# Kernel optimization log

Hardware: AMD Instinct MI355X
Metric: run time of the kernel (lower is better)

Reference implementation:

```python
import jax, jax.numpy as jnp
import numpy as np

B, S, D, H = 4, 2048, 1024, 16
HD = D // H  # head_dim = 64


def setup_inputs() -> dict:
    key = jax.random.key(0)
    ks = jax.random.split(key, 5)
    scale = 1.0 / np.sqrt(D)  # xavier-ish
    return {
        "query": jax.random.normal(ks[0], (B, S, D), dtype=jnp.float32),
        "Wq": jax.random.normal(ks[1], (D, D), dtype=jnp.float32) * scale,
        "bq": jnp.zeros((D,), dtype=jnp.float32),
        "Wk": jax.random.normal(ks[2], (D, D), dtype=jnp.float32) * scale,
        "bk": jnp.zeros((D,), dtype=jnp.float32),
        "Wv": jax.random.normal(ks[3], (D, D), dtype=jnp.float32) * scale,
        "bv": jnp.zeros((D,), dtype=jnp.float32),
        "Wo": jax.random.normal(ks[4], (D, D), dtype=jnp.float32) * scale,
        "bo": jnp.zeros((D,), dtype=jnp.float32),
    }


def reference(query, Wq, bq, Wk, bk, Wv, bv, Wo, bo):
    # Self-attention: key = value = query. Linear layers use y = x @ W^T + b (torch nn.Linear).
    q = query @ Wq.T + bq
    k = query @ Wk.T + bk
    v = query @ Wv.T + bv
    # [B, S, D] -> [B, H, S, HD]
    q = q.reshape(B, S, H, HD).transpose(0, 2, 1, 3)
    k = k.reshape(B, S, H, HD).transpose(0, 2, 1, 3)
    v = v.reshape(B, S, H, HD).transpose(0, 2, 1, 3)
    scores = jnp.einsum('bhqd,bhkd->bhqk', q, k) / jnp.sqrt(jnp.float32(HD))
    attn = jax.nn.softmax(scores, axis=-1)  # dropout=0 (eval)
    out = jnp.einsum('bhqk,bhkd->bhqd', attn, v)
    out = out.transpose(0, 2, 1, 3).reshape(B, S, D)
    out = out @ Wo.T + bo
    return out
```

## Files before the change

### kernel.cpp

```cpp
#include <hip/hip_runtime.h>
#include <cstdint>


#define B_ 4
#define S_ 2048
#define D_ 1024
#define H_ 16
#define HD_ 64
#define QKV_N 3072
#define QK_LD 2048
#define SCALE_Q 0.18033688011111772f

typedef __bf16 bf16x8 __attribute__((ext_vector_type(8)));
typedef __bf16 bf16x2 __attribute__((ext_vector_type(2)));
typedef float f32x4 __attribute__((ext_vector_type(4)));
typedef short short8 __attribute__((ext_vector_type(8)));

__device__ __forceinline__ unsigned short f2bf(float f) {
  unsigned int u = __builtin_bit_cast(unsigned int, f);
  u = (u + 0x7FFFu + ((u >> 16) & 1u)) >> 16;
  return (unsigned short)u;
}

__device__ __forceinline__ unsigned int pkbf(float a, float b) {
  bf16x2 v;
  v.x = (__bf16)a;
  v.y = (__bf16)b;
  return __builtin_bit_cast(unsigned int, v);
}

__device__ __forceinline__ void gload16(const void* g, void* l) {
  __builtin_amdgcn_global_load_lds(
      (const __attribute__((address_space(1))) void*)g,
      (__attribute__((address_space(3))) void*)l, 16, 0, 0);
}

__global__ __launch_bounds__(256) void cvt_all(
    const float* __restrict__ x, const float* __restrict__ w0, const float* __restrict__ w1,
    const float* __restrict__ w2, const float* __restrict__ w3,
    const float* __restrict__ bq, const float* __restrict__ bk, const float* __restrict__ bv,
    unsigned short* __restrict__ xb, unsigned short* __restrict__ wcat,
    float* __restrict__ bcat) {
  const int blk = blockIdx.x;
  const int t = threadIdx.x;
  if (blk < 4096) {
    size_t i = (size_t)blk * 256 + t;
    const float4* p = (const float4*)x + i * 2;
    float4 a = p[0], b = p[1];
    unsigned short o[8] = {f2bf(a.x), f2bf(a.y), f2bf(a.z), f2bf(a.w),
                           f2bf(b.x), f2bf(b.y), f2bf(b.z), f2bf(b.w)};
    *(uint4*)(xb + i * 8) = *(const uint4*)o;
  } else if (blk < 6144) {
    int y = (blk - 4096) >> 9;
    const float* src = (y == 0) ? w0 : (y == 1) ? w1 : (y == 2) ? w2 : w3;
    float s = (y == 0) ? SCALE_Q : 1.0f;
    size_t i = (size_t)((blk - 4096) & 511) * 256 + t;
    const float4* p = (const float4*)src + i * 2;
    float4 a = p[0], b = p[1];
    unsigned short o[8] = {f2bf(a.x * s), f2bf(a.y * s), f2bf(a.z * s), f2bf(a.w * s),
                           f2bf(b.x * s), f2bf(b.y * s), f2bf(b.z * s), f2bf(b.w * s)};
    *(uint4*)(wcat + (size_t)y * 1048576 + i * 8) = *(const uint4*)o;
  } else {
    for (int i = t; i < 3072; i += 256) {
      float v = (i < 1024) ? bq[i] * SCALE_Q : (i < 2048) ? bk[i - 1024] : bv[i - 2048];
      bcat[i] = v;
    }
  }
}

__device__ __forceinline__ void ld_afrag(const unsigned short* s, int rowbase, int quad,
                                         int sw, bf16x8 af[4][2]) {
#pragma unroll
  for (int mi2 = 0; mi2 < 4; ++mi2) {
    int row = rowbase + mi2 * 16;
#pragma unroll
    for (int kk = 0; kk < 2; ++kk)
      af[mi2][kk] = *(const bf16x8*)&s[row * 64 + ((((kk << 2) + quad) ^ sw) << 3)];
  }
}

__device__ __forceinline__ void ld_bfrag(const unsigned short* s, int rowbase, int quad,
                                         int sw, bf16x8 bf[2][2]) {
#pragma unroll
  for (int ni2 = 0; ni2 < 2; ++ni2) {
    int row = rowbase + ni2 * 16;
#pragma unroll
    for (int kk = 0; kk < 2; ++kk)
      bf[ni2][kk] = *(const bf16x8*)&s[row * 64 + ((((kk << 2) + quad) ^ sw) << 3)];
  }
}

#define SBAR() __builtin_amdgcn_sched_barrier(0)
#define BARRIER()                      \
  do {                                 \
    SBAR();                            \
    __builtin_amdgcn_s_barrier();      \
    SBAR();                            \
  } while (0)
#define WAITLGKM()                                      \
  do {                                                  \
    asm volatile("s_waitcnt lgkmcnt(0)" ::: "memory");  \
    SBAR();                                             \
  } while (0)

#define MM(qm, qn, BF)                                                                   \
  _Pragma("unroll") for (int mi2 = 0; mi2 < 4; ++mi2)                                    \
  _Pragma("unroll") for (int ni2 = 0; ni2 < 2; ++ni2)                                    \
  _Pragma("unroll") for (int kk = 0; kk < 2; ++kk)                                       \
      acc[(qm) * 4 + mi2][(qn) * 2 + ni2] = __builtin_amdgcn_mfma_f32_16x16x32_bf16(     \
          af[mi2][kk], BF[ni2][kk], acc[(qm) * 4 + mi2][(qn) * 2 + ni2], 0, 0, 0);

__global__ __launch_bounds__(512, 2) void gemm_qkv_256(
    const unsigned short* __restrict__ A, const unsigned short* __restrict__ W,
    const float* __restrict__ bias, unsigned short* __restrict__ qk,
    unsigned short* __restrict__ vt) {
  __shared__ __attribute__((aligned(16))) unsigned short sA[2][256 * 64];
  __shared__ __attribute__((aligned(16))) unsigned short sB[2][256 * 64];

  const int t = threadIdx.x;
  const int lane = t & 63;
  const int w = t >> 6;
  const int lm = lane & 15;
  const int quad = lane >> 4;
  const int sw = lm & 7;
  const int wm = (w >> 2) * 128;
  const int wn = (w & 3) * 64;

  const int bid = blockIdx.x;
  const int xcd = bid & 7, lin = bid >> 3;
  const int mt = xcd * 4 + (lin & 3);
  const int nt = lin >> 2;
  const int m0 = mt * 256, n0 = nt * 256;
  const int K = 1024;

  const int srow = t >> 3;
  const int scol = ((t & 7) ^ ((t >> 3) & 7)) << 3;
  const unsigned short* Ab = A + ((size_t)m0 + srow) * K + scol;
  const unsigned short* Wb = W + ((size_t)n0 + srow) * K + scol;

#define STG_A(bb, q, kt) gload16(Ab + (size_t)((q) * 64) * K + (kt), &sA[bb][(q) * 4096 + w * 512])
#define STG_B(bb, q, kt) gload16(Wb + (size_t)((q) * 64) * K + (kt), &sB[bb][(q) * 4096 + w * 512])

  STG_A(0, 0, 0); STG_A(0, 1, 0); STG_A(0, 2, 0); STG_A(0, 3, 0);
  STG_B(0, 0, 0); STG_B(0, 1, 0); STG_B(0, 2, 0); STG_B(0, 3, 0);
  STG_A(1, 0, 64); STG_A(1, 2, 64);
  STG_B(1, 0, 64); STG_B(1, 1, 64);
  STG_A(1, 1, 64); STG_A(1, 3, 64);
  asm volatile("s_waitcnt vmcnt(6)" ::: "memory");
  BARRIER();

  f32x4 acc[8][4] = {};
  bf16x8 af[4][2], bf0[2][2], bf1[2][2];

#define GROUP(c, kn1, kn2)                                                            \
  do {                                                                                \
    ld_afrag(sA[c], wm + lm, quad, sw, af);                                           \
    ld_bfrag(sB[c], wn + lm, quad, sw, bf0);                                          \
    STG_B(c ^ 1, 2, kn1);                                                             \
    STG_B(c ^ 1, 3, kn1);                                                             \
    BARRIER(); WAITLGKM();                                                            \
    __builtin_amdgcn_s_setprio(1); MM(0, 0, bf0); __builtin_amdgcn_s_setprio(0);      \
    BARRIER();                                                                        \
    ld_bfrag(sB[c], wn + 32 + lm, quad, sw, bf1);                                     \
    STG_A(c, 0, kn2);                                                                 \
    STG_A(c, 2, kn2);                                                                 \
    BARRIER(); WAITLGKM();                                                            \
    __builtin_amdgcn_s_setprio(1); MM(0, 1, bf1); __builtin_amdgcn_s_setprio(0);      \
    BARRIER();                                                                        \
    ld_afrag(sA[c], wm + 64 + lm, quad, sw, af);                                      \
    STG_B(c, 0, kn2);                                                                 \
    STG_B(c, 1, kn2);                                                                 \
    BARRIER(); WAITLGKM();                                                            \
    __builtin_amdgcn_s_setprio(1); MM(1, 0, bf0); __builtin_amdgcn_s_setprio(0);      \
    BARRIER();                                                                        \
    STG_A(c, 1, kn2);                                                                 \
    STG_A(c, 3, kn2);                                                                 \
    asm volatile("s_waitcnt vmcnt(6)" ::: "memory");                                  \
    BARRIER();                                                                        \
    __builtin_amdgcn_s_setprio(1); MM(1, 1, bf1); __builtin_amdgcn_s_setprio(0);      \
    BARRIER();                                                                        \
  } while (0)

  for (int kt = 0; kt < K; kt += 128) {
    const int kn1a = kt + 64;
    const int kn2a = (kt + 128 < K) ? kt + 128 : K - 64;
    const int kn1b = kn2a;
    const int kn2b = (kt + 192 < K) ? kt + 192 : K - 64;
    GROUP(0, kn1a, kn2a);
    GROUP(1, kn1b, kn2b);
  }

  asm volatile("s_waitcnt vmcnt(0)" ::: "memory");

#pragma unroll
  for (int mi = 0; mi < 8; ++mi) {
    const int rbase = m0 + wm + mi * 16 + quad * 4;
#pragma unroll
    for (int ni = 0; ni < 4; ++ni) {
      const int col = n0 + wn + ni * 16 + lm;
      const float bv = bias[col];
      float v0 = acc[mi][ni][0] + bv, v1 = acc[mi][ni][1] + bv;
      float v2 = acc[mi][ni][2] + bv, v3 = acc[mi][ni][3] + bv;
      if (n0 < 2048) {
        qk[(size_t)(rbase + 0) * QK_LD + col] = f2bf(v0);
        qk[(size_t)(rbase + 1) * QK_LD + col] = f2bf(v1);
        qk[(size_t)(rbase + 2) * QK_LD + col] = f2bf(v2);
        qk[(size_t)(rbase + 3) * QK_LD + col] = f2bf(v3);
      } else {
        int c2 = col - 2048;
        int bh = (m0 >> 11) * 16 + (c2 >> 6);
        int hd = c2 & 63;
        int sbase = rbase & 2047;
        uint2 pk = {pkbf(v0, v1), pkbf(v2, v3)};
        *(uint2*)(vt + (size_t)bh * (HD_ * S_) + (size_t)hd * S_ + sbase) = pk;
      }
    }
  }
}

__global__ __launch_bounds__(256) void gemm_bt(
    const unsigned short* __restrict__ A, const unsigned short* __restrict__ W,
    const float* __restrict__ bias, void* __restrict__ Cout,
    unsigned short* __restrict__ vt, int M, int N, int K, int mode) {
  __shared__ __attribute__((aligned(16))) unsigned short sA[128 * 32];
  __shared__ __attribute__((aligned(16))) unsigned short sB[128 * 32];
  const int t = threadIdx.x;
  const int lane = t & 63;
  const int w = t >> 6;
  const int lm = lane & 15;
  const int quad = lane >> 4;
  const int m0 = blockIdx.x * 128;
  const int n0 = blockIdx.y * 128;
  const int wm = (w & 1) * 64;
  const int wn = (w >> 1) * 64;

  const int off0 = t * 8, off1 = t * 8 + 2048;
  const int ar0 = off0 >> 5, ac0 = (((off0 >> 3) & 3) ^ ((ar0 >> 1) & 3)) * 8;
  const int ar1 = off1 >> 5, ac1 = (((off1 >> 3) & 3) ^ ((ar1 >> 1) & 3)) * 8;
  const unsigned short* Ag0 = A + (size_t)(m0 + ar0) * K + ac0;
  const unsigned short* Ag1 = A + (size_t)(m0 + ar1) * K + ac1;
  const unsigned short* Wg0 = W + (size_t)(n0 + ar0) * K + ac0;
  const unsigned short* Wg1 = W + (size_t)(n0 + ar1) * K + ac1;
  unsigned short* sA0 = &sA[w * 512];
  unsigned short* sA1 = &sA[2048 + w * 512];
  unsigned short* sB0 = &sB[w * 512];
  unsigned short* sB1 = &sB[2048 + w * 512];

  f32x4 acc[4][4] = {};

  for (int kt = 0; kt < K; kt += 32) {
    gload16(Ag0 + kt, sA0);
    gload16(Ag1 + kt, sA1);
    gload16(Wg0 + kt, sB0);
    gload16(Wg1 + kt, sB1);
    __syncthreads();
    bf16x8 af[4], bf[4];
#pragma unroll
    for (int mi = 0; mi < 4; ++mi) {
      int row = wm + mi * 16 + lm;
      af[mi] = *(const bf16x8*)&sA[row * 32 + ((quad ^ ((row >> 1) & 3)) << 3)];
    }
#pragma unroll
    for (int ni = 0; ni < 4; ++ni) {
      int row = wn + ni * 16 + lm;
      bf[ni] = *(const bf16x8*)&sB[row * 32 + ((quad ^ ((row >> 1) & 3)) << 3)];
    }
#pragma unroll
    for (int mi = 0; mi < 4; ++mi)
#pragma unroll
      for (int ni = 0; ni < 4; ++ni)
        acc[mi][ni] = __builtin_amdgcn_mfma_f32_16x16x32_bf16(af[mi], bf[ni], acc[mi][ni], 0, 0, 0);
    __syncthreads();
  }

#pragma unroll
  for (int mi = 0; mi < 4; ++mi)
#pragma unroll
    for (int ni = 0; ni < 4; ++ni) {
      int col = n0 + wn + ni * 16 + lm;
      float bv = bias[col];
      float v0 = acc[mi][ni][0] + bv, v1 = acc[mi][ni][1] + bv;
      float v2 = acc[mi][ni][2] + bv, v3 = acc[mi][ni][3] + bv;
      int rbase = m0 + wm + mi * 16 + quad * 4;
      if (mode == 0) {
        float* op = (float*)Cout;
        op[(size_t)(rbase + 0) * N + col] = v0;
        op[(size_t)(rbase + 1) * N + col] = v1;
        op[(size_t)(rbase + 2) * N + col] = v2;
        op[(size_t)(rbase + 3) * N + col] = v3;
      } else if (col < 2048) {
        unsigned short* op = (unsigned short*)Cout;
        op[(size_t)(rbase + 0) * QK_LD + col] = f2bf(v0);
        op[(size_t)(rbase + 1) * QK_LD + col] = f2bf(v1);
        op[(size_t)(rbase + 2) * QK_LD + col] = f2bf(v2);
        op[(size_t)(rbase + 3) * QK_LD + col] = f2bf(v3);
      } else {
        int c = col - 2048;
        int bh = (m0 >> 11) * 16 + (c >> 6);
        int hd = c & 63;
        int sbase = (rbase & 2047);
        uint2 pk = {pkbf(v0, v1), pkbf(v2, v3)};
        *(uint2*)(vt + (size_t)bh * (HD_ * S_) + (size_t)hd * S_ + sbase) = pk;
      }
    }
}

__global__ __launch_bounds__(512, 4) void attn_kernel(
    const unsigned short* __restrict__ qk, const unsigned short* __restrict__ vt,
    unsigned short* __restrict__ ab) {
  __shared__ __attribute__((aligned(16))) unsigned short sK[2][64 * 64];
  __shared__ __attribute__((aligned(16))) unsigned short sV[2][64 * 64];
  __shared__ __attribute__((aligned(16))) unsigned short sP[8][32 * 64];

  const int t = threadIdx.x;
  const int lane = t & 63;
  const int w = t >> 6;
  const int lm = lane & 15;
  const int quad = lane >> 4;
  const int bh = blockIdx.x & 63;
  const int b = bh >> 4, h = bh & 15;
  const int q0 = (blockIdx.x >> 6) * 256;

  const unsigned short* qg = qk + (size_t)b * S_ * QK_LD + h * HD_;
  const unsigned short* kg = qg + 1024;
  const unsigned short* vg = vt + (size_t)bh * HD_ * S_;

  const int r0 = t >> 3;
  const int c0 = ((t & 7) ^ (r0 & 7)) * 8;

  gload16(kg + (size_t)r0 * QK_LD + c0, &sK[0][w * 512]);
  gload16(vg + (size_t)r0 * S_ + c0, &sV[0][w * 512]);

  bf16x8 qf[2][2];
#pragma unroll
  for (int mi = 0; mi < 2; ++mi) {
    int row = q0 + w * 32 + mi * 16 + lm;
#pragma unroll
    for (int kc = 0; kc < 2; ++kc)
      qf[mi][kc] = *(const bf16x8*)(qg + (size_t)row * QK_LD + kc * 32 + quad * 8);
  }
  __syncthreads();

  unsigned short* sPw = sP[w];
  const bf16x8 ones = __builtin_bit_cast(bf16x8, (short8)(short)0x3F80);
  f32x4 o[2][4] = {};
  f32x4 Lacc[2] = {};

  for (int n0 = 0; n0 < S_; n0 += 64) {
    const int cur = (n0 >> 6) & 1, nxt = cur ^ 1;
    if (n0 + 64 < S_) {
      gload16(kg + (size_t)(n0 + 64 + r0) * QK_LD + c0, &sK[nxt][w * 512]);
      gload16(vg + (size_t)r0 * S_ + (n0 + 64) + c0, &sV[nxt][w * 512]);
    }

    f32x4 s[2][4] = {};
#pragma unroll
    for (int kc = 0; kc < 2; ++kc)
#pragma unroll
      for (int nb = 0; nb < 4; ++nb) {
        int row = nb * 16 + lm;
        bf16x8 kf = *(const bf16x8*)&sK[cur][row * 64 + (((kc * 4 + quad) ^ (row & 7)) << 3)];
#pragma unroll
        for (int mi = 0; mi < 2; ++mi)
          s[mi][nb] = __builtin_amdgcn_mfma_f32_16x16x32_bf16(kf, qf[mi][kc], s[mi][nb], 0, 0, 0);
      }

#pragma unroll
    for (int mi = 0; mi < 2; ++mi) {
      int prow = mi * 16 + lm;
      char* rowp = (char*)sPw + prow * 128;
#pragma unroll
      for (int nb = 0; nb < 4; ++nb) {
        const f32x4& sv = s[mi][nb];
        uint2 pk = {pkbf(__builtin_amdgcn_exp2f(sv[0]), __builtin_amdgcn_exp2f(sv[1])),
                    pkbf(__builtin_amdgcn_exp2f(sv[2]), __builtin_amdgcn_exp2f(sv[3]))};
        int c16 = (nb * 2 + (quad >> 1)) ^ (prow & 7);
        *(uint2*)(rowp + (c16 << 4) + ((quad & 1) << 3)) = pk;
      }
    }

#pragma unroll
    for (int kc = 0; kc < 2; ++kc) {
      bf16x8 pf[2];
#pragma unroll
      for (int mi = 0; mi < 2; ++mi) {
        int prow = mi * 16 + lm;
        pf[mi] = *(const bf16x8*)&sPw[prow * 64 + (((kc * 4 + quad) ^ (prow & 7)) << 3)];
        Lacc[mi] = __builtin_amdgcn_mfma_f32_16x16x32_bf16(pf[mi], ones, Lacc[mi], 0, 0, 0);
      }
#pragma unroll
      for (int nf = 0; nf < 4; ++nf) {
        int row = nf * 16 + lm;
        bf16x8 vf = *(const bf16x8*)&sV[cur][row * 64 + (((kc * 4 + quad) ^ (row & 7)) << 3)];
#pragma unroll
        for (int mi = 0; mi < 2; ++mi)
          o[mi][nf] = __builtin_amdgcn_mfma_f32_16x16x32_bf16(pf[mi], vf, o[mi][nf], 0, 0, 0);
      }
    }
    __syncthreads();
  }

#pragma unroll
  for (int mi = 0; mi < 2; ++mi)
#pragma unroll
    for (int r = 0; r < 4; ++r) {
      float rinv = 1.0f / Lacc[mi][r];
      int row = q0 + w * 32 + mi * 16 + quad * 4 + r;
#pragma unroll
      for (int nf = 0; nf < 4; ++nf) {
        int col = h * HD_ + nf * 16 + lm;
        ab[(size_t)(b * S_ + row) * D_ + col] = f2bf(o[mi][nf][r] * rinv);
      }
    }
}

extern "C" void kernel_launch(void* const* d_in, const int* in_sizes, int n_in,
                              void* d_out, int out_size, void* d_ws, size_t ws_size,
                              hipStream_t stream) {
  const float* x = (const float*)d_in[0];
  const float* Wq = (const float*)d_in[1];
  const float* bq = (const float*)d_in[2];
  const float* Wk = (const float*)d_in[3];
  const float* bk = (const float*)d_in[4];
  const float* Wv = (const float*)d_in[5];
  const float* bv = (const float*)d_in[6];
  const float* Wo = (const float*)d_in[7];
  const float* bo = (const float*)d_in[8];
  float* out = (float*)d_out;

  const size_t E = (size_t)B_ * S_ * D_;
  const size_t WE = (size_t)D_ * D_;
  unsigned short* xb = (unsigned short*)d_ws;
  unsigned short* wcat = xb + E;
  unsigned short* wob = wcat + 3 * WE;
  float* bcat = (float*)(wcat + 4 * WE);
  unsigned short* qkb = (unsigned short*)(bcat + 4096);
  unsigned short* vtb = qkb + (size_t)B_ * S_ * QK_LD;
  unsigned short* abuf = xb;

  cvt_all<<<dim3(6145), 256, 0, stream>>>(x, Wq, Wk, Wv, Wo, bq, bk, bv, xb, wcat, bcat);

  gemm_qkv_256<<<dim3(384), 512, 0, stream>>>(xb, wcat, bcat, qkb, vtb);
  attn_kernel<<<dim3(512), 512, 0, stream>>>(qkb, vtb, abuf);
  gemm_bt<<<dim3((B_ * S_) / 128, D_ / 128), 256, 0, stream>>>(
      abuf, wob, bo, out, nullptr, B_ * S_, D_, D_, 0);
}
```

Before: 276.7 us.

## Retile QKV GEMM from 256x256 to 128x384 block tiles

Changes the fused QKV projection GEMM's block tile from 256x256 to 128 rows by 384 columns, with per-wave tiles of 64x96 and a reorganised load/MFMA pipeline. The grid grows from 384 to 512 blocks, which may fill the GPU's compute units more evenly. The epilogue now picks between the Q/K and V^T output paths per column, because a 384-wide tile can straddle the boundary at column 2048. In exchange, each block reuses the A tile across fewer rows and moves a different amount of global traffic per FLOP.

```diff
diff --git a/kernel.cpp b/kernel.cpp
--- a/kernel.cpp
+++ b/kernel.cpp
@@ -68,28 +68,6 @@
   }
 }
 
-__device__ __forceinline__ void ld_afrag(const unsigned short* s, int rowbase, int quad,
-                                         int sw, bf16x8 af[4][2]) {
-#pragma unroll
-  for (int mi2 = 0; mi2 < 4; ++mi2) {
-    int row = rowbase + mi2 * 16;
-#pragma unroll
-    for (int kk = 0; kk < 2; ++kk)
-      af[mi2][kk] = *(const bf16x8*)&s[row * 64 + ((((kk << 2) + quad) ^ sw) << 3)];
-  }
-}
-
-__device__ __forceinline__ void ld_bfrag(const unsigned short* s, int rowbase, int quad,
-                                         int sw, bf16x8 bf[2][2]) {
-#pragma unroll
-  for (int ni2 = 0; ni2 < 2; ++ni2) {
-    int row = rowbase + ni2 * 16;
-#pragma unroll
-    for (int kk = 0; kk < 2; ++kk)
-      bf[ni2][kk] = *(const bf16x8*)&s[row * 64 + ((((kk << 2) + quad) ^ sw) << 3)];
-  }
-}
-
 #define SBAR() __builtin_amdgcn_sched_barrier(0)
 #define BARRIER()                      \
   do {                                 \
@@ -103,19 +81,41 @@
     SBAR();                                             \
   } while (0)
 
-#define MM(qm, qn, BF)                                                                   \
-  _Pragma("unroll") for (int mi2 = 0; mi2 < 4; ++mi2)                                    \
-  _Pragma("unroll") for (int ni2 = 0; ni2 < 2; ++ni2)                                    \
+__device__ __forceinline__ void ld_af2(const unsigned short* s, int rowbase, int quad,
+                                       int sw, bf16x8 af[2][2]) {
+#pragma unroll
+  for (int mi2 = 0; mi2 < 2; ++mi2) {
+    int row = rowbase + mi2 * 16;
+#pragma unroll
+    for (int kk = 0; kk < 2; ++kk)
+      af[mi2][kk] = *(const bf16x8*)&s[row * 64 + ((((kk << 2) + quad) ^ sw) << 3)];
+  }
+}
+
+__device__ __forceinline__ void ld_bf3(const unsigned short* s, int rowbase, int quad,
+                                       int sw, bf16x8 bf[3][2]) {
+#pragma unroll
+  for (int ni2 = 0; ni2 < 3; ++ni2) {
+    int row = rowbase + ni2 * 16;
+#pragma unroll
+    for (int kk = 0; kk < 2; ++kk)
+      bf[ni2][kk] = *(const bf16x8*)&s[row * 64 + ((((kk << 2) + quad) ^ sw) << 3)];
+  }
+}
+
+#define MMQ(qm, half, BF)                                                                \
+  _Pragma("unroll") for (int mi2 = 0; mi2 < 2; ++mi2)                                    \
+  _Pragma("unroll") for (int ni2 = 0; ni2 < 3; ++ni2)                                    \
   _Pragma("unroll") for (int kk = 0; kk < 2; ++kk)                                       \
-      acc[(qm) * 4 + mi2][(qn) * 2 + ni2] = __builtin_amdgcn_mfma_f32_16x16x32_bf16(     \
-          af[mi2][kk], BF[ni2][kk], acc[(qm) * 4 + mi2][(qn) * 2 + ni2], 0, 0, 0);
-
-__global__ __launch_bounds__(512, 2) void gemm_qkv_256(
+      acc[(qm) * 2 + mi2][(half) * 3 + ni2] = __builtin_amdgcn_mfma_f32_16x16x32_bf16(   \
+          af[mi2][kk], BF[ni2][kk], acc[(qm) * 2 + mi2][(half) * 3 + ni2], 0, 0, 0);
+
+__global__ __launch_bounds__(512, 2) void gemm_qkv_384(
     const unsigned short* __restrict__ A, const unsigned short* __restrict__ W,
     const float* __restrict__ bias, unsigned short* __restrict__ qk,
     unsigned short* __restrict__ vt) {
-  __shared__ __attribute__((aligned(16))) unsigned short sA[2][256 * 64];
-  __shared__ __attribute__((aligned(16))) unsigned short sB[2][256 * 64];
+  __shared__ __attribute__((aligned(16))) unsigned short sA[2][128 * 64];
+  __shared__ __attribute__((aligned(16))) unsigned short sB[2][384 * 64];
 
   const int t = threadIdx.x;
   const int lane = t & 63;
@@ -123,14 +123,14 @@
   const int lm = lane & 15;
   const int quad = lane >> 4;
   const int sw = lm & 7;
-  const int wm = (w >> 2) * 128;
-  const int wn = (w & 3) * 64;
+  const int wm = (w >> 2) * 64;
+  const int wn = (w & 3) * 96;
 
   const int bid = blockIdx.x;
   const int xcd = bid & 7, lin = bid >> 3;
-  const int mt = xcd * 4 + (lin & 3);
-  const int nt = lin >> 2;
-  const int m0 = mt * 256, n0 = nt * 256;
+  const int mt = xcd * 8 + (lin & 7);
+  const int nt = lin >> 3;
+  const int m0 = mt * 128, n0 = nt * 384;
   const int K = 1024;
 
   const int srow = t >> 3;
@@ -138,46 +138,51 @@
   const unsigned short* Ab = A + ((size_t)m0 + srow) * K + scol;
   const unsigned short* Wb = W + ((size_t)n0 + srow) * K + scol;
 
-#define STG_A(bb, q, kt) gload16(Ab + (size_t)((q) * 64) * K + (kt), &sA[bb][(q) * 4096 + w * 512])
-#define STG_B(bb, q, kt) gload16(Wb + (size_t)((q) * 64) * K + (kt), &sB[bb][(q) * 4096 + w * 512])
-
-  STG_A(0, 0, 0); STG_A(0, 1, 0); STG_A(0, 2, 0); STG_A(0, 3, 0);
-  STG_B(0, 0, 0); STG_B(0, 1, 0); STG_B(0, 2, 0); STG_B(0, 3, 0);
-  STG_A(1, 0, 64); STG_A(1, 2, 64);
-  STG_B(1, 0, 64); STG_B(1, 1, 64);
-  STG_A(1, 1, 64); STG_A(1, 3, 64);
+#define QSTG_A(bb, q, kt) gload16(Ab + (size_t)((q) * 64) * K + (kt), &sA[bb][(q) * 4096 + w * 512])
+#define QSTG_B(bb, q, kt) gload16(Wb + (size_t)((q) * 64) * K + (kt), &sB[bb][(q) * 4096 + w * 512])
+
+  QSTG_A(0, 0, 0); QSTG_A(0, 1, 0);
+  QSTG_B(0, 0, 0); QSTG_B(0, 1, 0); QSTG_B(0, 2, 0);
+  QSTG_B(0, 3, 0); QSTG_B(0, 4, 0); QSTG_B(0, 5, 0);
+  QSTG_B(1, 0, 64); QSTG_B(1, 1, 64);
+  QSTG_A(1, 0, 64); QSTG_A(1, 1, 64);
+  QSTG_B(1, 2, 64); QSTG_B(1, 3, 64);
   asm volatile("s_waitcnt vmcnt(6)" ::: "memory");
   BARRIER();
 
-  f32x4 acc[8][4] = {};
-  bf16x8 af[4][2], bf0[2][2], bf1[2][2];
-
-#define GROUP(c, kn1, kn2)                                                            \
+  f32x4 acc[4][6] = {};
+  bf16x8 af[2][2], bf0[3][2], bf1[3][2];
+
+#define QGROUP(c, kn1, kn2)                                                           \
   do {                                                                                \
-    ld_afrag(sA[c], wm + lm, quad, sw, af);                                           \
-    ld_bfrag(sB[c], wn + lm, quad, sw, bf0);                                          \
-    STG_B(c ^ 1, 2, kn1);                                                             \
-    STG_B(c ^ 1, 3, kn1);                                                             \
+                                                                \
+    ld_af2(sA[c], wm + lm, quad, sw, af);                                             \
+    ld_bf3(sB[c], wn + lm, quad, sw, bf0);                                            \
+    QSTG_B(c ^ 1, 4, kn1);                                                            \
+    QSTG_B(c ^ 1, 5, kn1);                                                            \
     BARRIER(); WAITLGKM();                                                            \
-    __builtin_amdgcn_s_setprio(1); MM(0, 0, bf0); __builtin_amdgcn_s_setprio(0);      \
+    __builtin_amdgcn_s_setprio(1); MMQ(0, 0, bf0); __builtin_amdgcn_s_setprio(0);     \
     BARRIER();                                                                        \
-    ld_bfrag(sB[c], wn + 32 + lm, quad, sw, bf1);                                     \
-    STG_A(c, 0, kn2);                                                                 \
-    STG_A(c, 2, kn2);                                                                 \
+                                                                \
+    ld_bf3(sB[c], wn + 48 + lm, quad, sw, bf1);                                       \
     BARRIER(); WAITLGKM();                                                            \
-    __builtin_amdgcn_s_setprio(1); MM(0, 1, bf1); __builtin_amdgcn_s_setprio(0);      \
+    __builtin_amdgcn_s_setprio(1); MMQ(0, 1, bf1); __builtin_amdgcn_s_setprio(0);     \
     BARRIER();                                                                        \
-    ld_afrag(sA[c], wm + 64 + lm, quad, sw, af);                                      \
-    STG_B(c, 0, kn2);                                                                 \
-    STG_B(c, 1, kn2);                                                                 \
+                                                                \
+    ld_af2(sA[c], wm + 32 + lm, quad, sw, af);                                        \
+    QSTG_B(c, 0, kn2);                                                                \
+    QSTG_B(c, 1, kn2);                                                                \
     BARRIER(); WAITLGKM();                                                            \
-    __builtin_amdgcn_s_setprio(1); MM(1, 0, bf0); __builtin_amdgcn_s_setprio(0);      \
+    __builtin_amdgcn_s_setprio(1); MMQ(1, 0, bf0); __builtin_amdgcn_s_setprio(0);     \
     BARRIER();                                                                        \
-    STG_A(c, 1, kn2);                                                                 \
-    STG_A(c, 3, kn2);                                                                 \
+                                                                \
+    QSTG_A(c, 0, kn2);                                                                \
+    QSTG_A(c, 1, kn2);                                                                \
+    QSTG_B(c, 2, kn2);                                                                \
+    QSTG_B(c, 3, kn2);                                                                \
     asm volatile("s_waitcnt vmcnt(6)" ::: "memory");                                  \
     BARRIER();                                                                        \
-    __builtin_amdgcn_s_setprio(1); MM(1, 1, bf1); __builtin_amdgcn_s_setprio(0);      \
+    __builtin_amdgcn_s_setprio(1); MMQ(1, 1, bf1); __builtin_amdgcn_s_setprio(0);     \
     BARRIER();                                                                        \
   } while (0)
 
@@ -186,22 +191,22 @@
     const int kn2a = (kt + 128 < K) ? kt + 128 : K - 64;
     const int kn1b = kn2a;
     const int kn2b = (kt + 192 < K) ? kt + 192 : K - 64;
-    GROUP(0, kn1a, kn2a);
-    GROUP(1, kn1b, kn2b);
+    QGROUP(0, kn1a, kn2a);
+    QGROUP(1, kn1b, kn2b);
   }
 
   asm volatile("s_waitcnt vmcnt(0)" ::: "memory");
 
 #pragma unroll
-  for (int mi = 0; mi < 8; ++mi) {
+  for (int mi = 0; mi < 4; ++mi) {
     const int rbase = m0 + wm + mi * 16 + quad * 4;
 #pragma unroll
-    for (int ni = 0; ni < 4; ++ni) {
+    for (int ni = 0; ni < 6; ++ni) {
       const int col = n0 + wn + ni * 16 + lm;
       const float bv = bias[col];
       float v0 = acc[mi][ni][0] + bv, v1 = acc[mi][ni][1] + bv;
       float v2 = acc[mi][ni][2] + bv, v3 = acc[mi][ni][3] + bv;
-      if (n0 < 2048) {
+      if (col < 2048) {
         qk[(size_t)(rbase + 0) * QK_LD + col] = f2bf(v0);
         qk[(size_t)(rbase + 1) * QK_LD + col] = f2bf(v1);
         qk[(size_t)(rbase + 2) * QK_LD + col] = f2bf(v2);
@@ -440,7 +445,7 @@
 
   cvt_all<<<dim3(6145), 256, 0, stream>>>(x, Wq, Wk, Wv, Wo, bq, bk, bv, xb, wcat, bcat);
 
-  gemm_qkv_256<<<dim3(384), 512, 0, stream>>>(xb, wcat, bcat, qkb, vtb);
+  gemm_qkv_384<<<dim3(512), 512, 0, stream>>>(xb, wcat, bcat, qkb, vtb);
   attn_kernel<<<dim3(512), 512, 0, stream>>>(qkb, vtb, abuf);
   gemm_bt<<<dim3((B_ * S_) / 128, D_ / 128), 256, 0, stream>>>(
       abuf, wob, bo, out, nullptr, B_ * S_, D_, D_, 0);
```

Result: faster. 262.6 us (-5.1%).
